# Kernel optimization log

Hardware: AMD Instinct MI355X
Metric: run time of the kernel (lower is better)

## Reference

```python
import jax, jax.numpy as jnp
import numpy as np

# Mesh/packing dims: deltaV_packed.view(B, M, V, ndims) requires N = B*M*V
B, M, V = 2, 4, 40000
N = B * M * V            # 320_000 packed vertices
E = 960000               # ~3 edges per vertex (triangle mesh)
F_IN = 128               # n_input_features
LAT = 128                # latent_channels
NDIMS = 3
N_HIDDEN = 2             # n_f2f_hidden_layer


def graph_conv(x, edges, W0, b0, W1, b1):
    """pytorch3d-style GraphConv: w0(x) + sum_{j in N(i)} w1(x_j), undirected edges."""
    h0 = x @ W0 + b0                     # self term  [N, out]
    h1 = x @ W1 + b1                     # neighbor messages [N, out]
    src, dst = edges[:, 0], edges[:, 1]
    agg = jnp.zeros_like(h0).at[src].add(h1[dst]).at[dst].add(h1[src])
    return h0 + agg


def setup_inputs() -> dict:
    key = jax.random.key(0)
    ks = jax.random.split(key, 20)
    inp = {
        "features": jax.random.normal(ks[0], (N, F_IN), jnp.float32),
        "edges": jax.random.randint(ks[1], (E, 2), 0, N, dtype=jnp.int32),
    }
    # Layer dims: f2f first (F_IN->LAT), 2 hidden (LAT->LAT), f2v (LAT->NDIMS).
    dims = [(F_IN, LAT), (LAT, LAT), (LAT, LAT), (LAT, NDIMS)]
    for i, (din, dout) in enumerate(dims):
        kk = jax.random.split(ks[2 + i], 4)
        s = 1.0 / np.sqrt(din)
        inp[f"W0_{i}"] = jax.random.normal(kk[0], (din, dout), jnp.float32) * s
        inp[f"b0_{i}"] = jnp.zeros((dout,), jnp.float32)
        inp[f"W1_{i}"] = jax.random.normal(kk[1], (din, dout), jnp.float32) * s
        inp[f"b1_{i}"] = jnp.zeros((dout,), jnp.float32)
    return inp


def reference(features, edges,
              W0_0, b0_0, W1_0, b1_0,
              W0_1, b0_1, W1_1, b1_1,
              W0_2, b0_2, W1_2, b1_2,
              W0_3, b0_3, W1_3, b1_3):
    # Features2FeaturesResidual: first GC + 2 hidden GCs (ReLU each, norm='none'),
    # residual skip (identity since F_IN == LAT).
    h = jax.nn.relu(graph_conv(features, edges, W0_0, b0_0, W1_0, b1_0))
    h = jax.nn.relu(graph_conv(h, edges, W0_1, b0_1, W1_1, b1_1))
    h = jax.nn.relu(graph_conv(h, edges, W0_2, b0_2, W1_2, b1_2))
    h = h + features
    # f2v: GC(latent -> ndims), no activation
    deltaV = graph_conv(h, edges, W0_3, b0_3, W1_3, b1_3)
    return deltaV.reshape(B, M, V, NDIMS)
```

## Files before the change

kernel.cpp:

```cpp
#include <hip/hip_runtime.h>
#include <hip/hip_bf16.h>

#define NNODES 320000
#define NEDGES 960000
#define NPART 8
#define PARTSZ (NNODES / NPART)

typedef __attribute__((ext_vector_type(8))) short short8;
typedef __attribute__((ext_vector_type(4))) float f32x4;

__device__ __forceinline__ float b2f(unsigned short u) {
    return __uint_as_float(((unsigned)u) << 16);
}
__device__ __forceinline__ unsigned short f2b(float f) {
    __hip_bfloat16 h = __float2bfloat16(f);
    union { __hip_bfloat16 h; unsigned short u; } cv;
    cv.h = h;
    return cv.u;
}


__global__ void k_zero(int* p, int n) {
    int i = blockIdx.x * blockDim.x + threadIdx.x;
    int s = gridDim.x * blockDim.x;
    for (; i < n; i += s) p[i] = 0;
}

__global__ void k_count(const int* __restrict__ edges, int* __restrict__ deg) {
    int r = blockIdx.x & (NPART - 1);
    int lo = r * PARTSZ, hi = lo + PARTSZ;
    int i = (blockIdx.x >> 3) * blockDim.x + threadIdx.x;
    int s = (gridDim.x >> 3) * blockDim.x;
    for (; i < NEDGES; i += s) {
        int2 e = *(const int2*)&edges[2 * i];
        if (e.x >= lo && e.x < hi) atomicAdd(&deg[e.x], 1);
        if (e.y >= lo && e.y < hi) atomicAdd(&deg[e.y], 1);
    }
}

#define SCAN_BLOCK 256
#define SCAN_ITEMS 8
#define SCAN_CHUNK 2048
#define SCAN_NB 157

__global__ void k_scan1(const int* __restrict__ deg, int* __restrict__ bsum) {
    __shared__ int sd[SCAN_BLOCK];
    int b = blockIdx.x, t = threadIdx.x;
    int base = b * SCAN_CHUNK + t * SCAN_ITEMS;
    int s = 0;
    for (int i = 0; i < SCAN_ITEMS; i++) {
        int g = base + i;
        if (g < NNODES) s += deg[g];
    }
    sd[t] = s;
    __syncthreads();
    for (int off = 128; off > 0; off >>= 1) {
        if (t < off) sd[t] += sd[t + off];
        __syncthreads();
    }
    if (t == 0) bsum[b] = sd[0];
}

__global__ void k_scan2(int* bsum, int* rowptr) {
    if (blockIdx.x == 0 && threadIdx.x == 0) {
        int run = 0;
        for (int b = 0; b < SCAN_NB; b++) {
            int v = bsum[b];
            bsum[b] = run;
            run += v;
        }
        rowptr[NNODES] = run;
    }
}

__global__ void k_scan3(int* __restrict__ deg_cursor, int* __restrict__ rowptr,
                        const int* __restrict__ bsum, float* __restrict__ degf) {
    __shared__ int sd[SCAN_BLOCK];
    int b = blockIdx.x, t = threadIdx.x;
    int base = b * SCAN_CHUNK + t * SCAN_ITEMS;
    int v[SCAN_ITEMS];
    int s = 0;
    for (int i = 0; i < SCAN_ITEMS; i++) {
        int g = base + i;
        v[i] = (g < NNODES) ? deg_cursor[g] : 0;
        s += v[i];
    }
    sd[t] = s;
    __syncthreads();
    for (int off = 1; off < SCAN_BLOCK; off <<= 1) {
        int x = (t >= off) ? sd[t - off] : 0;
        __syncthreads();
        sd[t] += x;
        __syncthreads();
    }
    int prefix = bsum[b] + (sd[t] - s);
    for (int i = 0; i < SCAN_ITEMS; i++) {
        int g = base + i;
        if (g < NNODES) {
            rowptr[g] = prefix;
            deg_cursor[g] = prefix;
            degf[g] = (float)v[i];
            prefix += v[i];
        }
    }
}

__global__ void k_fill(const int* __restrict__ edges, int* __restrict__ cursor,
                       int* __restrict__ adj) {
    int r = blockIdx.x & (NPART - 1);
    int lo = r * PARTSZ, hi = lo + PARTSZ;
    int i = (blockIdx.x >> 3) * blockDim.x + threadIdx.x;
    int s = (gridDim.x >> 3) * blockDim.x;
    for (; i < NEDGES; i += s) {
        int2 e = *(const int2*)&edges[2 * i];
        if (e.x >= lo && e.x < hi) adj[atomicAdd(&cursor[e.x], 1)] = e.y;
        if (e.y >= lo && e.y < hi) adj[atomicAdd(&cursor[e.y], 1)] = e.x;
    }
}


__global__ void k_cvt(const float* __restrict__ f, unsigned short* __restrict__ o,
                      long n4) {
    long i = (long)blockIdx.x * blockDim.x + threadIdx.x;
    long s = (long)gridDim.x * blockDim.x;
    for (; i < n4; i += s) {
        float4 v = *(const float4*)&f[i * 4];
        uint2 u;
        u.x = (unsigned)f2b(v.x) | ((unsigned)f2b(v.y) << 16);
        u.y = (unsigned)f2b(v.z) | ((unsigned)f2b(v.w) << 16);
        *(uint2*)&o[i * 4] = u;
    }
}

__global__ void k_cvtW(const float* __restrict__ W0, const float* __restrict__ W1,
                       unsigned short* __restrict__ Wt) {
    int idx = blockIdx.x * blockDim.x + threadIdx.x;
    if (idx >= 128 * 256) return;
    int c = idx >> 8, k = idx & 255;
    float v = (k < 128) ? W0[k * 128 + c] : W1[(k - 128) * 128 + c];
    Wt[idx] = f2b(v);
}


template <int L>
__global__ __launch_bounds__(256) void k_gather(
    const unsigned short* __restrict__ x, const int* __restrict__ rowptr,
    const int* __restrict__ adj, unsigned short* __restrict__ xsum) {
    int wid = (blockIdx.x * blockDim.x + threadIdx.x) >> 6;
    int lane = threadIdx.x & 63;
    int nw = (gridDim.x * blockDim.x) >> 6;
    int r = lane >> 4;
    int cb = (lane & 15) * 8;
    for (int node = wid; node < NNODES; node += nw) {
        int s = rowptr[node], e = rowptr[node + 1];
        float a[8];
#pragma unroll
        for (int q = 0; q < 8; q++) a[q] = 0.f;
        for (int p = s; p < e; p += 8) {
            int i0 = p + r, i1 = p + r + 4;
            uint4 v0 = make_uint4(0, 0, 0, 0), v1 = make_uint4(0, 0, 0, 0);
            if (i0 < e) {
                int j = adj[i0];
                v0 = *(const uint4*)&x[(size_t)j * 128 + cb];
            }
            if (i1 < e) {
                int j = adj[i1];
                v1 = *(const uint4*)&x[(size_t)j * 128 + cb];
            }
            unsigned w0[4] = {v0.x, v0.y, v0.z, v0.w};
            unsigned w1[4] = {v1.x, v1.y, v1.z, v1.w};
#pragma unroll
            for (int q = 0; q < 4; q++) {
                a[2 * q] += b2f(w0[q] & 0xffff) + b2f(w1[q] & 0xffff);
                a[2 * q + 1] += b2f(w0[q] >> 16) + b2f(w1[q] >> 16);
            }
        }
#pragma unroll
        for (int q = 0; q < 8; q++) a[q] += __shfl_xor(a[q], 16, 64);
#pragma unroll
        for (int q = 0; q < 8; q++) a[q] += __shfl_xor(a[q], 32, 64);
        if (lane < 16) {
            uint4 o;
            o.x = (unsigned)f2b(a[0]) | ((unsigned)f2b(a[1]) << 16);
            o.y = (unsigned)f2b(a[2]) | ((unsigned)f2b(a[3]) << 16);
            o.z = (unsigned)f2b(a[4]) | ((unsigned)f2b(a[5]) << 16);
            o.w = (unsigned)f2b(a[6]) | ((unsigned)f2b(a[7]) << 16);
            *(uint4*)&xsum[(size_t)node * 128 + cb] = o;
        }
    }
}


#define XLD 136

template <int RES, int L>
__global__ __launch_bounds__(512, 4) void k_gemmF(
    const unsigned short* x, const unsigned short* __restrict__ xsum,
    const unsigned short* __restrict__ Wt, const float* __restrict__ b0,
    const float* __restrict__ b1, const float* __restrict__ degf,
    const unsigned short* __restrict__ feat, unsigned short* out) {
    __shared__ __align__(16) unsigned short Xs[64 * XLD];
    __shared__ __align__(16) unsigned short Ss[64 * XLD];

    int tid = threadIdx.x;
    int wave = tid >> 6, lane = tid & 63;
    int wm = wave >> 2, wn = wave & 3;
    int kg = (lane >> 4) << 3;
    int cl = lane & 15;

    short8 bF[8][2];
#pragma unroll
    for (int ks = 0; ks < 8; ++ks)
#pragma unroll
        for (int nf = 0; nf < 2; ++nf) {
            int c = wn * 32 + nf * 16 + cl;
            bF[ks][nf] = *(const short8*)&Wt[(size_t)c * 256 + ks * 32 + kg];
        }

    int rowBase = blockIdx.x * 64;
#pragma unroll
    for (int it = 0; it < 2; ++it) {
        int e = (it * 512 + tid) * 8;
        int r = e >> 7, k = e & 127;
        *(uint4*)&Xs[r * XLD + k] = *(const uint4*)&x[(size_t)(rowBase + r) * 128 + k];
        *(uint4*)&Ss[r * XLD + k] =
            *(const uint4*)&xsum[(size_t)(rowBase + r) * 128 + k];
    }
    __syncthreads();

    f32x4 acc[2][2];
#pragma unroll
    for (int i = 0; i < 2; i++)
#pragma unroll
        for (int j = 0; j < 2; j++) acc[i][j] = (f32x4){0.f, 0.f, 0.f, 0.f};

#pragma unroll
    for (int ks = 0; ks < 8; ++ks) {
        const unsigned short* src = (ks < 4) ? Xs : Ss;
        int kk = (ks & 3) * 32 + kg;
        short8 aF[2];
#pragma unroll
        for (int mf = 0; mf < 2; ++mf) {
            int r = wm * 32 + mf * 16 + cl;
            aF[mf] = *(const short8*)&src[r * XLD + kk];
        }
#pragma unroll
        for (int mf = 0; mf < 2; mf++)
#pragma unroll
            for (int nf = 0; nf < 2; nf++)
                acc[mf][nf] = __builtin_amdgcn_mfma_f32_16x16x32_bf16(
                    aF[mf], bF[ks][nf], acc[mf][nf], 0, 0, 0);
    }

#pragma unroll
    for (int nf = 0; nf < 2; nf++) {
        int c = wn * 32 + nf * 16 + cl;
        float bias0 = b0[c], bias1 = b1[c];
#pragma unroll
        for (int mf = 0; mf < 2; mf++) {
            int r0 = rowBase + wm * 32 + mf * 16 + ((lane >> 4) << 2);
            f32x4 d = acc[mf][nf];
#pragma unroll
            for (int q = 0; q < 4; q++) {
                int r = r0 + q;
                float v = d[q] + bias0 + degf[r] * bias1;
                v = fmaxf(v, 0.f);
                if (RES) v += b2f(feat[(size_t)r * 128 + c]);
                out[(size_t)r * 128 + c] = f2b(v);
            }
        }
    }
}


__global__ __launch_bounds__(256) void k_fin(
    const unsigned short* __restrict__ act, const unsigned short* __restrict__ hsum,
    const float* __restrict__ W0, const float* __restrict__ W1,
    const float* __restrict__ b0, const float* __restrict__ b1,
    const float* __restrict__ degf, float* __restrict__ out) {
    __shared__ __align__(16) unsigned short xa[64 * XLD];
    __shared__ __align__(16) unsigned short xs2[64 * XLD];
    __shared__ float Wf[768];
    __shared__ float ps[64][4][4];

    int tid = threadIdx.x;
    int nodeBase = blockIdx.x * 64;

    for (int idx = tid; idx < 384; idx += 256) {
        Wf[idx] = W0[idx];
        Wf[384 + idx] = W1[idx];
    }
#pragma unroll
    for (int it = 0; it < 4; ++it) {
        int e = (it * 256 + tid) * 8;
        int r = e >> 7, k = e & 127;
        *(uint4*)&xa[r * XLD + k] = *(const uint4*)&act[(size_t)(nodeBase + r) * 128 + k];
        *(uint4*)&xs2[r * XLD + k] =
            *(const uint4*)&hsum[(size_t)(nodeBase + r) * 128 + k];
    }
    __syncthreads();

    int n = tid >> 2, q = tid & 3;
    const unsigned short* src = (q < 2) ? xa : xs2;
    int kloc = (q & 1) * 64;
    float a0 = 0.f, a1 = 0.f, a2 = 0.f;
#pragma unroll
    for (int kk = 0; kk < 64; kk += 8) {
        uint4 v = *(const uint4*)&src[n * XLD + kloc + kk];
        unsigned vv[4] = {v.x, v.y, v.z, v.w};
#pragma unroll
        for (int t = 0; t < 4; t++) {
            int kgl = q * 64 + kk + 2 * t;
            float x0 = b2f(vv[t] & 0xffff), x1 = b2f(vv[t] >> 16);
            const float* w = &Wf[kgl * 3];
            a0 += x0 * w[0] + x1 * w[3];
            a1 += x0 * w[1] + x1 * w[4];
            a2 += x0 * w[2] + x1 * w[5];
        }
    }
    ps[n][q][0] = a0;
    ps[n][q][1] = a1;
    ps[n][q][2] = a2;
    __syncthreads();
    if (q == 0) {
        int node = nodeBase + n;
        float dg = degf[node];
#pragma unroll
        for (int c = 0; c < 3; c++) {
            float d = ps[n][0][c] + ps[n][1][c] + ps[n][2][c] + ps[n][3][c] +
                      b0[c] + dg * b1[c];
            out[(size_t)node * 3 + c] = d;
        }
    }
}


extern "C" void kernel_launch(void* const* d_in, const int* in_sizes, int n_in,
                              void* d_out, int out_size, void* d_ws, size_t ws_size,
                              hipStream_t stream) {
    const float* features = (const float*)d_in[0];
    const int* edges = (const int*)d_in[1];
    const float *W0[4], *B0[4], *W1[4], *B1[4];
    for (int i = 0; i < 4; i++) {
        W0[i] = (const float*)d_in[2 + 4 * i];
        B0[i] = (const float*)d_in[3 + 4 * i];
        W1[i] = (const float*)d_in[4 + 4 * i];
        B1[i] = (const float*)d_in[5 + 4 * i];
    }

    char* p = (char*)d_ws;
    auto alloc = [&](size_t bytes) {
        void* r = (void*)p;
        p += (bytes + 255) & ~(size_t)255;
        return r;
    };
    int* rowptr = (int*)alloc((NNODES + 1) * sizeof(int));
    int* cursor = (int*)alloc((NNODES + 1) * sizeof(int));
    float* degf = (float*)alloc(NNODES * sizeof(float));
    int* adj = (int*)alloc((size_t)2 * NEDGES * sizeof(int));
    int* bsum = (int*)alloc(1024);
    unsigned short* feat_bf = (unsigned short*)alloc((size_t)NNODES * 128 * 2);
    unsigned short* act = (unsigned short*)alloc((size_t)NNODES * 128 * 2);
    unsigned short* xsum = (unsigned short*)alloc((size_t)NNODES * 128 * 2);
    unsigned short* Wtb = (unsigned short*)alloc((size_t)3 * 128 * 256 * 2);

    k_zero<<<1024, 256, 0, stream>>>(cursor, NNODES + 1);
    k_count<<<2048, 256, 0, stream>>>(edges, cursor);
    k_scan1<<<SCAN_NB, SCAN_BLOCK, 0, stream>>>(cursor, bsum);
    k_scan2<<<1, 64, 0, stream>>>(bsum, rowptr);
    k_scan3<<<SCAN_NB, SCAN_BLOCK, 0, stream>>>(cursor, rowptr, bsum, degf);
    k_fill<<<2048, 256, 0, stream>>>(edges, cursor, adj);

    k_cvt<<<2048, 256, 0, stream>>>(features, feat_bf, (long)NNODES * 128 / 4);
    for (int l = 0; l < 3; l++)
        k_cvtW<<<128, 256, 0, stream>>>(W0[l], W1[l], Wtb + (size_t)l * 128 * 256);

    k_gather<0><<<8192, 256, 0, stream>>>(feat_bf, rowptr, adj, xsum);
    k_gemmF<0, 0><<<NNODES / 64, 512, 0, stream>>>(feat_bf, xsum, Wtb, B0[0], B1[0],
                                                   degf, nullptr, act);
    k_gather<1><<<8192, 256, 0, stream>>>(act, rowptr, adj, xsum);
    k_gemmF<0, 1><<<NNODES / 64, 512, 0, stream>>>(act, xsum, Wtb + 128 * 256, B0[1],
                                                   B1[1], degf, nullptr, act);
    k_gather<2><<<8192, 256, 0, stream>>>(act, rowptr, adj, xsum);
    k_gemmF<1, 2><<<NNODES / 64, 512, 0, stream>>>(act, xsum, Wtb + 2 * 128 * 256,
                                                   B0[2], B1[2], degf, feat_bf, act);
    k_gather<3><<<8192, 256, 0, stream>>>(act, rowptr, adj, xsum);
    k_fin<<<NNODES / 64, 256, 0, stream>>>(act, xsum, W0[3], W1[3], B0[3], B1[3],
                                           degf, (float*)d_out);
}
```

Before: 1.153 ms.

## Fuse neighbor gather into per-layer GEMM kernels via shared-memory aggregation

Each layer's neighbor-sum gather now runs inside the GEMM kernel. Waves aggregate neighbor rows for their tile's nodes directly into shared memory, so the separate xsum round-trip through global memory and the extra launches go away. The same is done for the final 3-output layer. Ping-pong activation buffers replace in-place writes, and the serial block-sum scan becomes a parallel shared-memory scan. The trade-off is that gather latency is no longer overlapped across many independent small blocks, only 8-16 nodes are serialized per wave, and weights are reloaded from global per tile.

Result: slower. 1.333 ms (+15.6%).

```diff
diff --git a/kernel.cpp b/kernel.cpp
--- a/kernel.cpp
+++ b/kernel.cpp
@@ -62,15 +62,19 @@
 }
 
 __global__ void k_scan2(int* bsum, int* rowptr) {
-    if (blockIdx.x == 0 && threadIdx.x == 0) {
-        int run = 0;
-        for (int b = 0; b < SCAN_NB; b++) {
-            int v = bsum[b];
-            bsum[b] = run;
-            run += v;
-        }
-        rowptr[NNODES] = run;
-    }
+    __shared__ int sd[256];
+    int t = threadIdx.x;
+    int v = (t < SCAN_NB) ? bsum[t] : 0;
+    sd[t] = v;
+    __syncthreads();
+    for (int off = 1; off < 256; off <<= 1) {
+        int x = (t >= off) ? sd[t - off] : 0;
+        __syncthreads();
+        sd[t] += x;
+        __syncthreads();
+    }
+    if (t < SCAN_NB) bsum[t] = sd[t] - v;
+    if (t == SCAN_NB - 1) rowptr[NNODES] = sd[t];
 }
 
 __global__ void k_scan3(int* __restrict__ deg_cursor, int* __restrict__ rowptr,
@@ -142,63 +146,15 @@
 }
 
 
-template <int L>
-__global__ __launch_bounds__(256) void k_gather(
-    const unsigned short* __restrict__ x, const int* __restrict__ rowptr,
-    const int* __restrict__ adj, unsigned short* __restrict__ xsum) {
-    int wid = (blockIdx.x * blockDim.x + threadIdx.x) >> 6;
-    int lane = threadIdx.x & 63;
-    int nw = (gridDim.x * blockDim.x) >> 6;
-    int r = lane >> 4;
-    int cb = (lane & 15) * 8;
-    for (int node = wid; node < NNODES; node += nw) {
-        int s = rowptr[node], e = rowptr[node + 1];
-        float a[8];
-#pragma unroll
-        for (int q = 0; q < 8; q++) a[q] = 0.f;
-        for (int p = s; p < e; p += 8) {
-            int i0 = p + r, i1 = p + r + 4;
-            uint4 v0 = make_uint4(0, 0, 0, 0), v1 = make_uint4(0, 0, 0, 0);
-            if (i0 < e) {
-                int j = adj[i0];
-                v0 = *(const uint4*)&x[(size_t)j * 128 + cb];
-            }
-            if (i1 < e) {
-                int j = adj[i1];
-                v1 = *(const uint4*)&x[(size_t)j * 128 + cb];
-            }
-            unsigned w0[4] = {v0.x, v0.y, v0.z, v0.w};
-            unsigned w1[4] = {v1.x, v1.y, v1.z, v1.w};
-#pragma unroll
-            for (int q = 0; q < 4; q++) {
-                a[2 * q] += b2f(w0[q] & 0xffff) + b2f(w1[q] & 0xffff);
-                a[2 * q + 1] += b2f(w0[q] >> 16) + b2f(w1[q] >> 16);
-            }
-        }
-#pragma unroll
-        for (int q = 0; q < 8; q++) a[q] += __shfl_xor(a[q], 16, 64);
-#pragma unroll
-        for (int q = 0; q < 8; q++) a[q] += __shfl_xor(a[q], 32, 64);
-        if (lane < 16) {
-            uint4 o;
-            o.x = (unsigned)f2b(a[0]) | ((unsigned)f2b(a[1]) << 16);
-            o.y = (unsigned)f2b(a[2]) | ((unsigned)f2b(a[3]) << 16);
-            o.z = (unsigned)f2b(a[4]) | ((unsigned)f2b(a[5]) << 16);
-            o.w = (unsigned)f2b(a[6]) | ((unsigned)f2b(a[7]) << 16);
-            *(uint4*)&xsum[(size_t)node * 128 + cb] = o;
-        }
-    }
-}
-
-
 #define XLD 136
 
 template <int RES, int L>
-__global__ __launch_bounds__(512, 4) void k_gemmF(
-    const unsigned short* x, const unsigned short* __restrict__ xsum,
-    const unsigned short* __restrict__ Wt, const float* __restrict__ b0,
-    const float* __restrict__ b1, const float* __restrict__ degf,
-    const unsigned short* __restrict__ feat, unsigned short* out) {
+__global__ __launch_bounds__(512, 4) void k_layer(
+    const unsigned short* __restrict__ xin, const int* __restrict__ rowptr,
+    const int* __restrict__ adj, const unsigned short* __restrict__ Wt,
+    const float* __restrict__ b0, const float* __restrict__ b1,
+    const float* __restrict__ degf, const unsigned short* __restrict__ feat,
+    unsigned short* __restrict__ out) {
     __shared__ __align__(16) unsigned short Xs[64 * XLD];
     __shared__ __align__(16) unsigned short Ss[64 * XLD];
 
@@ -207,129 +163,216 @@
     int wm = wave >> 2, wn = wave & 3;
     int kg = (lane >> 4) << 3;
     int cl = lane & 15;
-
-    short8 bF[8][2];
-#pragma unroll
-    for (int ks = 0; ks < 8; ++ks)
-#pragma unroll
-        for (int nf = 0; nf < 2; ++nf) {
+    int slot = lane >> 4;
+    int cb = cl * 8;
+
+    for (int tile = blockIdx.x; tile < NNODES / 64; tile += gridDim.x) {
+        int rowBase = tile * 64;
+        __syncthreads();
+
+#pragma unroll
+        for (int it = 0; it < 2; ++it) {
+            int e = (it * 512 + tid) * 8;
+            int r = e >> 7, k = e & 127;
+            *(uint4*)&Xs[r * XLD + k] =
+                *(const uint4*)&xin[(size_t)(rowBase + r) * 128 + k];
+        }
+
+        for (int nl = 0; nl < 8; ++nl) {
+            int nodeLocal = wave * 8 + nl;
+            int node = rowBase + nodeLocal;
+            int s = rowptr[node], e = rowptr[node + 1];
+            float a[8];
+#pragma unroll
+            for (int q = 0; q < 8; q++) a[q] = 0.f;
+            for (int p = s; p < e; p += 8) {
+                int i0 = p + slot, i1 = p + slot + 4;
+                uint4 v0 = make_uint4(0, 0, 0, 0), v1 = make_uint4(0, 0, 0, 0);
+                if (i0 < e) {
+                    int j = adj[i0];
+                    v0 = *(const uint4*)&xin[(size_t)j * 128 + cb];
+                }
+                if (i1 < e) {
+                    int j = adj[i1];
+                    v1 = *(const uint4*)&xin[(size_t)j * 128 + cb];
+                }
+                unsigned w0[4] = {v0.x, v0.y, v0.z, v0.w};
+                unsigned w1[4] = {v1.x, v1.y, v1.z, v1.w};
+#pragma unroll
+                for (int q = 0; q < 4; q++) {
+                    a[2 * q] += b2f(w0[q] & 0xffff) + b2f(w1[q] & 0xffff);
+                    a[2 * q + 1] += b2f(w0[q] >> 16) + b2f(w1[q] >> 16);
+                }
+            }
+#pragma unroll
+            for (int q = 0; q < 8; q++) a[q] += __shfl_xor(a[q], 16, 64);
+#pragma unroll
+            for (int q = 0; q < 8; q++) a[q] += __shfl_xor(a[q], 32, 64);
+            if (lane < 16) {
+                uint4 o;
+                o.x = (unsigned)f2b(a[0]) | ((unsigned)f2b(a[1]) << 16);
+                o.y = (unsigned)f2b(a[2]) | ((unsigned)f2b(a[3]) << 16);
+                o.z = (unsigned)f2b(a[4]) | ((unsigned)f2b(a[5]) << 16);
+                o.w = (unsigned)f2b(a[6]) | ((unsigned)f2b(a[7]) << 16);
+                *(uint4*)&Ss[nodeLocal * XLD + cb] = o;
+            }
+        }
+        __syncthreads();
+
+        f32x4 acc[2][2];
+#pragma unroll
+        for (int i = 0; i < 2; i++)
+#pragma unroll
+            for (int j = 0; j < 2; j++) acc[i][j] = (f32x4){0.f, 0.f, 0.f, 0.f};
+
+#pragma unroll
+        for (int ks = 0; ks < 8; ++ks) {
+            const unsigned short* src = (ks < 4) ? Xs : Ss;
+            int kk = (ks & 3) * 32 + kg;
+            short8 aF[2];
+#pragma unroll
+            for (int mf = 0; mf < 2; ++mf) {
+                int r = wm * 32 + mf * 16 + cl;
+                aF[mf] = *(const short8*)&src[r * XLD + kk];
+            }
+#pragma unroll
+            for (int nf = 0; nf < 2; nf++) {
+                int c = wn * 32 + nf * 16 + cl;
+                short8 bF = *(const short8*)&Wt[(size_t)c * 256 + ks * 32 + kg];
+#pragma unroll
+                for (int mf = 0; mf < 2; mf++)
+                    acc[mf][nf] = __builtin_amdgcn_mfma_f32_16x16x32_bf16(
+                        aF[mf], bF, acc[mf][nf], 0, 0, 0);
+            }
+        }
+
+#pragma unroll
+        for (int nf = 0; nf < 2; nf++) {
             int c = wn * 32 + nf * 16 + cl;
-            bF[ks][nf] = *(const short8*)&Wt[(size_t)c * 256 + ks * 32 + kg];
-        }
-
-    int rowBase = blockIdx.x * 64;
-#pragma unroll
-    for (int it = 0; it < 2; ++it) {
-        int e = (it * 512 + tid) * 8;
-        int r = e >> 7, k = e & 127;
-        *(uint4*)&Xs[r * XLD + k] = *(const uint4*)&x[(size_t)(rowBase + r) * 128 + k];
-        *(uint4*)&Ss[r * XLD + k] =
-            *(const uint4*)&xsum[(size_t)(rowBase + r) * 128 + k];
-    }
-    __syncthreads();
-
-    f32x4 acc[2][2];
-#pragma unroll
-    for (int i = 0; i < 2; i++)
-#pragma unroll
-        for (int j = 0; j < 2; j++) acc[i][j] = (f32x4){0.f, 0.f, 0.f, 0.f};
-
-#pragma unroll
-    for (int ks = 0; ks < 8; ++ks) {
-        const unsigned short* src = (ks < 4) ? Xs : Ss;
-        int kk = (ks & 3) * 32 + kg;
-        short8 aF[2];
-#pragma unroll
-        for (int mf = 0; mf < 2; ++mf) {
-            int r = wm * 32 + mf * 16 + cl;
-            aF[mf] = *(const short8*)&src[r * XLD + kk];
-        }
-#pragma unroll
-        for (int mf = 0; mf < 2; mf++)
-#pragma unroll
-            for (int nf = 0; nf < 2; nf++)
-                acc[mf][nf] = __builtin_amdgcn_mfma_f32_16x16x32_bf16(
-                    aF[mf], bF[ks][nf], acc[mf][nf], 0, 0, 0);
-    }
-
-#pragma unroll
-    for (int nf = 0; nf < 2; nf++) {
-        int c = wn * 32 + nf * 16 + cl;
-        float bias0 = b0[c], bias1 = b1[c];
-#pragma unroll
-        for (int mf = 0; mf < 2; mf++) {
-            int r0 = rowBase + wm * 32 + mf * 16 + ((lane >> 4) << 2);
-            f32x4 d = acc[mf][nf];
-#pragma unroll
-            for (int q = 0; q < 4; q++) {
-                int r = r0 + q;
-                float v = d[q] + bias0 + degf[r] * bias1;
-                v = fmaxf(v, 0.f);
-                if (RES) v += b2f(feat[(size_t)r * 128 + c]);
-                out[(size_t)r * 128 + c] = f2b(v);
-            }
-        }
-    }
-}
-
-
-__global__ __launch_bounds__(256) void k_fin(
-    const unsigned short* __restrict__ act, const unsigned short* __restrict__ hsum,
-    const float* __restrict__ W0, const float* __restrict__ W1,
-    const float* __restrict__ b0, const float* __restrict__ b1,
-    const float* __restrict__ degf, float* __restrict__ out) {
+            float bias0 = b0[c], bias1 = b1[c];
+#pragma unroll
+            for (int mf = 0; mf < 2; mf++) {
+                int r0 = rowBase + wm * 32 + mf * 16 + ((lane >> 4) << 2);
+                f32x4 d = acc[mf][nf];
+#pragma unroll
+                for (int q = 0; q < 4; q++) {
+                    int r = r0 + q;
+                    float v = d[q] + bias0 + degf[r] * bias1;
+                    v = fmaxf(v, 0.f);
+                    if (RES) v += b2f(feat[(size_t)r * 128 + c]);
+                    out[(size_t)r * 128 + c] = f2b(v);
+                }
+            }
+        }
+    }
+}
+
+
+__global__ __launch_bounds__(256) void k_finF(
+    const unsigned short* __restrict__ act, const int* __restrict__ rowptr,
+    const int* __restrict__ adj, const float* __restrict__ W0,
+    const float* __restrict__ W1, const float* __restrict__ b0,
+    const float* __restrict__ b1, const float* __restrict__ degf,
+    float* __restrict__ out) {
     __shared__ __align__(16) unsigned short xa[64 * XLD];
     __shared__ __align__(16) unsigned short xs2[64 * XLD];
     __shared__ float Wf[768];
     __shared__ float ps[64][4][4];
 
     int tid = threadIdx.x;
-    int nodeBase = blockIdx.x * 64;
+    int wave = tid >> 6, lane = tid & 63;
+    int slot = lane >> 4;
+    int cb = (lane & 15) * 8;
 
     for (int idx = tid; idx < 384; idx += 256) {
         Wf[idx] = W0[idx];
         Wf[384 + idx] = W1[idx];
     }
-#pragma unroll
-    for (int it = 0; it < 4; ++it) {
-        int e = (it * 256 + tid) * 8;
-        int r = e >> 7, k = e & 127;
-        *(uint4*)&xa[r * XLD + k] = *(const uint4*)&act[(size_t)(nodeBase + r) * 128 + k];
-        *(uint4*)&xs2[r * XLD + k] =
-            *(const uint4*)&hsum[(size_t)(nodeBase + r) * 128 + k];
-    }
-    __syncthreads();
-
-    int n = tid >> 2, q = tid & 3;
-    const unsigned short* src = (q < 2) ? xa : xs2;
-    int kloc = (q & 1) * 64;
-    float a0 = 0.f, a1 = 0.f, a2 = 0.f;
-#pragma unroll
-    for (int kk = 0; kk < 64; kk += 8) {
-        uint4 v = *(const uint4*)&src[n * XLD + kloc + kk];
-        unsigned vv[4] = {v.x, v.y, v.z, v.w};
-#pragma unroll
-        for (int t = 0; t < 4; t++) {
-            int kgl = q * 64 + kk + 2 * t;
-            float x0 = b2f(vv[t] & 0xffff), x1 = b2f(vv[t] >> 16);
-            const float* w = &Wf[kgl * 3];
-            a0 += x0 * w[0] + x1 * w[3];
-            a1 += x0 * w[1] + x1 * w[4];
-            a2 += x0 * w[2] + x1 * w[5];
-        }
-    }
-    ps[n][q][0] = a0;
-    ps[n][q][1] = a1;
-    ps[n][q][2] = a2;
-    __syncthreads();
-    if (q == 0) {
-        int node = nodeBase + n;
-        float dg = degf[node];
-#pragma unroll
-        for (int c = 0; c < 3; c++) {
-            float d = ps[n][0][c] + ps[n][1][c] + ps[n][2][c] + ps[n][3][c] +
-                      b0[c] + dg * b1[c];
-            out[(size_t)node * 3 + c] = d;
+
+    for (int tile = blockIdx.x; tile < NNODES / 64; tile += gridDim.x) {
+        int nodeBase = tile * 64;
+        __syncthreads();
+
+#pragma unroll
+        for (int it = 0; it < 4; ++it) {
+            int e = (it * 256 + tid) * 8;
+            int r = e >> 7, k = e & 127;
+            *(uint4*)&xa[r * XLD + k] =
+                *(const uint4*)&act[(size_t)(nodeBase + r) * 128 + k];
+        }
+
+        for (int nl = 0; nl < 16; ++nl) {
+            int nodeLocal = wave * 16 + nl;
+            int node = nodeBase + nodeLocal;
+            int s = rowptr[node], e = rowptr[node + 1];
+            float a[8];
+#pragma unroll
+            for (int q = 0; q < 8; q++) a[q] = 0.f;
+            for (int p = s; p < e; p += 8) {
+                int i0 = p + slot, i1 = p + slot + 4;
+                uint4 v0 = make_uint4(0, 0, 0, 0), v1 = make_uint4(0, 0, 0, 0);
+                if (i0 < e) {
+                    int j = adj[i0];
+                    v0 = *(const uint4*)&act[(size_t)j * 128 + cb];
+                }
+                if (i1 < e) {
+                    int j = adj[i1];
+                    v1 = *(const uint4*)&act[(size_t)j * 128 + cb];
+                }
+                unsigned w0[4] = {v0.x, v0.y, v0.z, v0.w};
+                unsigned w1[4] = {v1.x, v1.y, v1.z, v1.w};
+#pragma unroll
+                for (int q = 0; q < 4; q++) {
+                    a[2 * q] += b2f(w0[q] & 0xffff) + b2f(w1[q] & 0xffff);
+                    a[2 * q + 1] += b2f(w0[q] >> 16) + b2f(w1[q] >> 16);
+                }
+            }
+#pragma unroll
+            for (int q = 0; q < 8; q++) a[q] += __shfl_xor(a[q], 16, 64);
+#pragma unroll
+            for (int q = 0; q < 8; q++) a[q] += __shfl_xor(a[q], 32, 64);
+            if (lane < 16) {
+                uint4 o;
+                o.x = (unsigned)f2b(a[0]) | ((unsigned)f2b(a[1]) << 16);
+                o.y = (unsigned)f2b(a[2]) | ((unsigned)f2b(a[3]) << 16);
+                o.z = (unsigned)f2b(a[4]) | ((unsigned)f2b(a[5]) << 16);
+                o.w = (unsigned)f2b(a[6]) | ((unsigned)f2b(a[7]) << 16);
+                *(uint4*)&xs2[nodeLocal * XLD + cb] = o;
+            }
+        }
+        __syncthreads();
+
+        int n = tid >> 2, q = tid & 3;
+        const unsigned short* src = (q < 2) ? xa : xs2;
+        int kloc = (q & 1) * 64;
+        float a0 = 0.f, a1 = 0.f, a2 = 0.f;
+#pragma unroll
+        for (int kk = 0; kk < 64; kk += 8) {
+            uint4 v = *(const uint4*)&src[n * XLD + kloc + kk];
+            unsigned vv[4] = {v.x, v.y, v.z, v.w};
+#pragma unroll
+            for (int t = 0; t < 4; t++) {
+                int kgl = q * 64 + kk + 2 * t;
+                float x0 = b2f(vv[t] & 0xffff), x1 = b2f(vv[t] >> 16);
+                const float* w = &Wf[kgl * 3];
+                a0 += x0 * w[0] + x1 * w[3];
+                a1 += x0 * w[1] + x1 * w[4];
+                a2 += x0 * w[2] + x1 * w[5];
+            }
+        }
+        ps[n][q][0] = a0;
+        ps[n][q][1] = a1;
+        ps[n][q][2] = a2;
+        __syncthreads();
+        if (q == 0) {
+            int node = nodeBase + n;
+            float dg = degf[node];
+#pragma unroll
+            for (int c = 0; c < 3; c++) {
+                float d = ps[n][0][c] + ps[n][1][c] + ps[n][2][c] + ps[n][3][c] +
+                          b0[c] + dg * b1[c];
+                out[(size_t)node * 3 + c] = d;
+            }
         }
     }
 }
@@ -360,14 +403,14 @@
     int* adj = (int*)alloc((size_t)2 * NEDGES * sizeof(int));
     int* bsum = (int*)alloc(1024);
     unsigned short* feat_bf = (unsigned short*)alloc((size_t)NNODES * 128 * 2);
-    unsigned short* act = (unsigned short*)alloc((size_t)NNODES * 128 * 2);
-    unsigned short* xsum = (unsigned short*)alloc((size_t)NNODES * 128 * 2);
+    unsigned short* actA = (unsigned short*)alloc((size_t)NNODES * 128 * 2);
+    unsigned short* actB = (unsigned short*)alloc((size_t)NNODES * 128 * 2);
     unsigned short* Wtb = (unsigned short*)alloc((size_t)3 * 128 * 256 * 2);
 
     k_zero<<<1024, 256, 0, stream>>>(cursor, NNODES + 1);
     k_count<<<2048, 256, 0, stream>>>(edges, cursor);
     k_scan1<<<SCAN_NB, SCAN_BLOCK, 0, stream>>>(cursor, bsum);
-    k_scan2<<<1, 64, 0, stream>>>(bsum, rowptr);
+    k_scan2<<<1, 256, 0, stream>>>(bsum, rowptr);
     k_scan3<<<SCAN_NB, SCAN_BLOCK, 0, stream>>>(cursor, rowptr, bsum, degf);
     k_fill<<<2048, 256, 0, stream>>>(edges, cursor, adj);
 
@@ -375,16 +418,12 @@
     for (int l = 0; l < 3; l++)
         k_cvtW<<<128, 256, 0, stream>>>(W0[l], W1[l], Wtb + (size_t)l * 128 * 256);
 
-    k_gather<0><<<8192, 256, 0, stream>>>(feat_bf, rowptr, adj, xsum);
-    k_gemmF<0, 0><<<NNODES / 64, 512, 0, stream>>>(feat_bf, xsum, Wtb, B0[0], B1[0],
-                                                   degf, nullptr, act);
-    k_gather<1><<<8192, 256, 0, stream>>>(act, rowptr, adj, xsum);
-    k_gemmF<0, 1><<<NNODES / 64, 512, 0, stream>>>(act, xsum, Wtb + 128 * 256, B0[1],
-                                                   B1[1], degf, nullptr, act);
-    k_gather<2><<<8192, 256, 0, stream>>>(act, rowptr, adj, xsum);
-    k_gemmF<1, 2><<<NNODES / 64, 512, 0, stream>>>(act, xsum, Wtb + 2 * 128 * 256,
-                                                   B0[2], B1[2], degf, feat_bf, act);
-    k_gather<3><<<8192, 256, 0, stream>>>(act, rowptr, adj, xsum);
-    k_fin<<<NNODES / 64, 256, 0, stream>>>(act, xsum, W0[3], W1[3], B0[3], B1[3],
-                                           degf, (float*)d_out);
-}
+    k_layer<0, 0><<<1250, 512, 0, stream>>>(feat_bf, rowptr, adj, Wtb, B0[0], B1[0],
+                                            degf, nullptr, actA);
+    k_layer<0, 1><<<1250, 512, 0, stream>>>(actA, rowptr, adj, Wtb + 128 * 256,
+                                            B0[1], B1[1], degf, nullptr, actB);
+    k_layer<1, 2><<<1250, 512, 0, stream>>>(actB, rowptr, adj, Wtb + 2 * 128 * 256,
+                                            B0[2], B1[2], degf, feat_bf, actA);
+    k_finF<<<2500, 256, 0, stream>>>(actA, rowptr, adj, W0[3], W1[3], B0[3], B1[3],
+                                     degf, (float*)d_out);
+}
```

## Make GEMM persistent with tile prefetch, gather two nodes per wave, parallelize scan

Applied to the files above, without the earlier changes.

The fused GEMM kernel becomes persistent: 1250 blocks loop over the 64-row tiles. Each block prefetches the next tile's x and xsum rows into registers while it computes the current one, and B fragments are now loaded inside the k-loop instead of held in registers. The neighbour-gather kernel processes two nodes per wave, which raises the number of independent memory loads in flight. The single-thread block-sum scan is replaced by a 256-thread shared-memory scan. In exchange, persistence reduces occupancy via launch bounds and re-reads weights per tile, and the scan assumes SCAN_NB is at most 256.

Result: no change. 1.169 ms (+1.4%).

```diff
diff --git a/kernel.cpp b/kernel.cpp
--- a/kernel.cpp
+++ b/kernel.cpp
@@ -62,15 +62,19 @@
 }
 
 __global__ void k_scan2(int* bsum, int* rowptr) {
-    if (blockIdx.x == 0 && threadIdx.x == 0) {
-        int run = 0;
-        for (int b = 0; b < SCAN_NB; b++) {
-            int v = bsum[b];
-            bsum[b] = run;
-            run += v;
-        }
-        rowptr[NNODES] = run;
-    }
+    __shared__ int sd[256];
+    int t = threadIdx.x;
+    int v = (t < SCAN_NB) ? bsum[t] : 0;
+    sd[t] = v;
+    __syncthreads();
+    for (int off = 1; off < 256; off <<= 1) {
+        int x = (t >= off) ? sd[t - off] : 0;
+        __syncthreads();
+        sd[t] += x;
+        __syncthreads();
+    }
+    if (t < SCAN_NB) bsum[t] = sd[t] - v;
+    if (t == SCAN_NB - 1) rowptr[NNODES] = sd[t];
 }
 
 __global__ void k_scan3(int* __restrict__ deg_cursor, int* __restrict__ rowptr,
@@ -149,52 +153,67 @@
     int wid = (blockIdx.x * blockDim.x + threadIdx.x) >> 6;
     int lane = threadIdx.x & 63;
     int nw = (gridDim.x * blockDim.x) >> 6;
-    int r = lane >> 4;
+    int slot = lane >> 4;
     int cb = (lane & 15) * 8;
-    for (int node = wid; node < NNODES; node += nw) {
-        int s = rowptr[node], e = rowptr[node + 1];
-        float a[8];
-#pragma unroll
-        for (int q = 0; q < 8; q++) a[q] = 0.f;
-        for (int p = s; p < e; p += 8) {
-            int i0 = p + r, i1 = p + r + 4;
-            uint4 v0 = make_uint4(0, 0, 0, 0), v1 = make_uint4(0, 0, 0, 0);
-            if (i0 < e) {
-                int j = adj[i0];
-                v0 = *(const uint4*)&x[(size_t)j * 128 + cb];
+    for (int n0 = wid * 2; n0 < NNODES; n0 += nw * 2) {
+        int s0 = rowptr[n0], e0 = rowptr[n0 + 1], e1 = rowptr[n0 + 2];
+        int d0 = e0 - s0, d1 = e1 - e0;
+        int dmax = d0 > d1 ? d0 : d1;
+        float a0[8], a1[8];
+#pragma unroll
+        for (int q = 0; q < 8; q++) { a0[q] = 0.f; a1[q] = 0.f; }
+        for (int p = 0; p < dmax; p += 8) {
+            int i00 = s0 + p + slot, i01 = i00 + 4;
+            int i10 = e0 + p + slot, i11 = i10 + 4;
+            uint4 v00 = make_uint4(0, 0, 0, 0), v01 = make_uint4(0, 0, 0, 0);
+            uint4 v10 = make_uint4(0, 0, 0, 0), v11 = make_uint4(0, 0, 0, 0);
+            if (i00 < e0) v00 = *(const uint4*)&x[(size_t)adj[i00] * 128 + cb];
+            if (i01 < e0) v01 = *(const uint4*)&x[(size_t)adj[i01] * 128 + cb];
+            if (i10 < e1) v10 = *(const uint4*)&x[(size_t)adj[i10] * 128 + cb];
+            if (i11 < e1) v11 = *(const uint4*)&x[(size_t)adj[i11] * 128 + cb];
+            unsigned w00[4] = {v00.x, v00.y, v00.z, v00.w};
+            unsigned w01[4] = {v01.x, v01.y, v01.z, v01.w};
+            unsigned w10[4] = {v10.x, v10.y, v10.z, v10.w};
+            unsigned w11[4] = {v11.x, v11.y, v11.z, v11.w};
+#pragma unroll
+            for (int q = 0; q < 4; q++) {
+                a0[2 * q] += b2f(w00[q] & 0xffff) + b2f(w01[q] & 0xffff);
+                a0[2 * q + 1] += b2f(w00[q] >> 16) + b2f(w01[q] >> 16);
+                a1[2 * q] += b2f(w10[q] & 0xffff) + b2f(w11[q] & 0xffff);
+                a1[2 * q + 1] += b2f(w10[q] >> 16) + b2f(w11[q] >> 16);
             }
-            if (i1 < e) {
-                int j = adj[i1];
-                v1 = *(const uint4*)&x[(size_t)j * 128 + cb];
-            }
-            unsigned w0[4] = {v0.x, v0.y, v0.z, v0.w};
-            unsigned w1[4] = {v1.x, v1.y, v1.z, v1.w};
-#pragma unroll
-            for (int q = 0; q < 4; q++) {
-                a[2 * q] += b2f(w0[q] & 0xffff) + b2f(w1[q] & 0xffff);
-                a[2 * q + 1] += b2f(w0[q] >> 16) + b2f(w1[q] >> 16);
-            }
-        }
-#pragma unroll
-        for (int q = 0; q < 8; q++) a[q] += __shfl_xor(a[q], 16, 64);
-#pragma unroll
-        for (int q = 0; q < 8; q++) a[q] += __shfl_xor(a[q], 32, 64);
-        if (lane < 16) {
+        }
+#pragma unroll
+        for (int q = 0; q < 8; q++) {
+            a0[q] += __shfl_xor(a0[q], 16, 64);
+            a1[q] += __shfl_xor(a1[q], 16, 64);
+        }
+#pragma unroll
+        for (int q = 0; q < 8; q++) {
+            a0[q] += __shfl_xor(a0[q], 32, 64);
+            a1[q] += __shfl_xor(a1[q], 32, 64);
+        }
+        float sel[8];
+#pragma unroll
+        for (int q = 0; q < 8; q++) sel[q] = (lane < 16) ? a0[q] : a1[q];
+        if (lane < 32) {
             uint4 o;
-            o.x = (unsigned)f2b(a[0]) | ((unsigned)f2b(a[1]) << 16);
-            o.y = (unsigned)f2b(a[2]) | ((unsigned)f2b(a[3]) << 16);
-            o.z = (unsigned)f2b(a[4]) | ((unsigned)f2b(a[5]) << 16);
-            o.w = (unsigned)f2b(a[6]) | ((unsigned)f2b(a[7]) << 16);
-            *(uint4*)&xsum[(size_t)node * 128 + cb] = o;
+            o.x = (unsigned)f2b(sel[0]) | ((unsigned)f2b(sel[1]) << 16);
+            o.y = (unsigned)f2b(sel[2]) | ((unsigned)f2b(sel[3]) << 16);
+            o.z = (unsigned)f2b(sel[4]) | ((unsigned)f2b(sel[5]) << 16);
+            o.w = (unsigned)f2b(sel[6]) | ((unsigned)f2b(sel[7]) << 16);
+            int dst = (lane < 16) ? n0 : (n0 + 1);
+            *(uint4*)&xsum[(size_t)dst * 128 + cb] = o;
         }
     }
 }
 
 
 #define XLD 136
+#define NT (NNODES / 64)
 
 template <int RES, int L>
-__global__ __launch_bounds__(512, 4) void k_gemmF(
+__global__ __launch_bounds__(512, 2) void k_gemmF(
     const unsigned short* x, const unsigned short* __restrict__ xsum,
     const unsigned short* __restrict__ Wt, const float* __restrict__ b0,
     const float* __restrict__ b1, const float* __restrict__ degf,
@@ -208,67 +227,86 @@
     int kg = (lane >> 4) << 3;
     int cl = lane & 15;
 
-    short8 bF[8][2];
-#pragma unroll
-    for (int ks = 0; ks < 8; ++ks)
-#pragma unroll
-        for (int nf = 0; nf < 2; ++nf) {
-            int c = wn * 32 + nf * 16 + cl;
-            bF[ks][nf] = *(const short8*)&Wt[(size_t)c * 256 + ks * 32 + kg];
-        }
-
-    int rowBase = blockIdx.x * 64;
-#pragma unroll
-    for (int it = 0; it < 2; ++it) {
-        int e = (it * 512 + tid) * 8;
-        int r = e >> 7, k = e & 127;
-        *(uint4*)&Xs[r * XLD + k] = *(const uint4*)&x[(size_t)(rowBase + r) * 128 + k];
-        *(uint4*)&Ss[r * XLD + k] =
-            *(const uint4*)&xsum[(size_t)(rowBase + r) * 128 + k];
-    }
-    __syncthreads();
-
-    f32x4 acc[2][2];
-#pragma unroll
-    for (int i = 0; i < 2; i++)
-#pragma unroll
-        for (int j = 0; j < 2; j++) acc[i][j] = (f32x4){0.f, 0.f, 0.f, 0.f};
-
-#pragma unroll
-    for (int ks = 0; ks < 8; ++ks) {
-        const unsigned short* src = (ks < 4) ? Xs : Ss;
-        int kk = (ks & 3) * 32 + kg;
-        short8 aF[2];
-#pragma unroll
-        for (int mf = 0; mf < 2; ++mf) {
-            int r = wm * 32 + mf * 16 + cl;
-            aF[mf] = *(const short8*)&src[r * XLD + kk];
-        }
-#pragma unroll
-        for (int mf = 0; mf < 2; mf++)
-#pragma unroll
-            for (int nf = 0; nf < 2; nf++)
-                acc[mf][nf] = __builtin_amdgcn_mfma_f32_16x16x32_bf16(
-                    aF[mf], bF[ks][nf], acc[mf][nf], 0, 0, 0);
-    }
-
+    float bias0[2], bias1[2];
 #pragma unroll
     for (int nf = 0; nf < 2; nf++) {
         int c = wn * 32 + nf * 16 + cl;
-        float bias0 = b0[c], bias1 = b1[c];
-#pragma unroll
-        for (int mf = 0; mf < 2; mf++) {
-            int r0 = rowBase + wm * 32 + mf * 16 + ((lane >> 4) << 2);
-            f32x4 d = acc[mf][nf];
-#pragma unroll
-            for (int q = 0; q < 4; q++) {
-                int r = r0 + q;
-                float v = d[q] + bias0 + degf[r] * bias1;
-                v = fmaxf(v, 0.f);
-                if (RES) v += b2f(feat[(size_t)r * 128 + c]);
-                out[(size_t)r * 128 + c] = f2b(v);
+        bias0[nf] = b0[c];
+        bias1[nf] = b1[c];
+    }
+
+    uint4 pa[2], ps[2];
+    auto loadTile = [&](int tile) {
+#pragma unroll
+        for (int it = 0; it < 2; ++it) {
+            int e = (it * 512 + tid) * 8;
+            int r = e >> 7, k = e & 127;
+            pa[it] = *(const uint4*)&x[(size_t)(tile * 64 + r) * 128 + k];
+            ps[it] = *(const uint4*)&xsum[(size_t)(tile * 64 + r) * 128 + k];
+        }
+    };
+
+    int tile = blockIdx.x;
+    if (tile < NT) loadTile(tile);
+    while (tile < NT) {
+        int next = tile + gridDim.x;
+        __syncthreads();
+#pragma unroll
+        for (int it = 0; it < 2; ++it) {
+            int e = (it * 512 + tid) * 8;
+            int r = e >> 7, k = e & 127;
+            *(uint4*)&Xs[r * XLD + k] = pa[it];
+            *(uint4*)&Ss[r * XLD + k] = ps[it];
+        }
+        __syncthreads();
+        if (next < NT) loadTile(next);
+
+        int rowBase = tile * 64;
+        f32x4 acc[2][2];
+#pragma unroll
+        for (int i = 0; i < 2; i++)
+#pragma unroll
+            for (int j = 0; j < 2; j++) acc[i][j] = (f32x4){0.f, 0.f, 0.f, 0.f};
+
+#pragma unroll
+        for (int ks = 0; ks < 8; ++ks) {
+            const unsigned short* src = (ks < 4) ? Xs : Ss;
+            int kk = (ks & 3) * 32 + kg;
+            short8 aF[2];
+#pragma unroll
+            for (int mf = 0; mf < 2; ++mf) {
+                int r = wm * 32 + mf * 16 + cl;
+                aF[mf] = *(const short8*)&src[r * XLD + kk];
             }
-        }
+#pragma unroll
+            for (int nf = 0; nf < 2; nf++) {
+                int c = wn * 32 + nf * 16 + cl;
+                short8 bF = *(const short8*)&Wt[(size_t)c * 256 + ks * 32 + kg];
+#pragma unroll
+                for (int mf = 0; mf < 2; mf++)
+                    acc[mf][nf] = __builtin_amdgcn_mfma_f32_16x16x32_bf16(
+                        aF[mf], bF, acc[mf][nf], 0, 0, 0);
+            }
+        }
+
+#pragma unroll
+        for (int nf = 0; nf < 2; nf++) {
+            int c = wn * 32 + nf * 16 + cl;
+#pragma unroll
+            for (int mf = 0; mf < 2; mf++) {
+                int r0 = rowBase + wm * 32 + mf * 16 + ((lane >> 4) << 2);
+                f32x4 d = acc[mf][nf];
+#pragma unroll
+                for (int q = 0; q < 4; q++) {
+                    int r = r0 + q;
+                    float v = d[q] + bias0[nf] + degf[r] * bias1[nf];
+                    v = fmaxf(v, 0.f);
+                    if (RES) v += b2f(feat[(size_t)r * 128 + c]);
+                    out[(size_t)r * 128 + c] = f2b(v);
+                }
+            }
+        }
+        tile = next;
     }
 }
 
@@ -367,7 +405,7 @@
     k_zero<<<1024, 256, 0, stream>>>(cursor, NNODES + 1);
     k_count<<<2048, 256, 0, stream>>>(edges, cursor);
     k_scan1<<<SCAN_NB, SCAN_BLOCK, 0, stream>>>(cursor, bsum);
-    k_scan2<<<1, 64, 0, stream>>>(bsum, rowptr);
+    k_scan2<<<1, 256, 0, stream>>>(bsum, rowptr);
     k_scan3<<<SCAN_NB, SCAN_BLOCK, 0, stream>>>(cursor, rowptr, bsum, degf);
     k_fill<<<2048, 256, 0, stream>>>(edges, cursor, adj);
 
@@ -376,14 +414,14 @@
         k_cvtW<<<128, 256, 0, stream>>>(W0[l], W1[l], Wtb + (size_t)l * 128 * 256);
 
     k_gather<0><<<8192, 256, 0, stream>>>(feat_bf, rowptr, adj, xsum);
-    k_gemmF<0, 0><<<NNODES / 64, 512, 0, stream>>>(feat_bf, xsum, Wtb, B0[0], B1[0],
-                                                   degf, nullptr, act);
+    k_gemmF<0, 0><<<1250, 512, 0, stream>>>(feat_bf, xsum, Wtb, B0[0], B1[0], degf,
+                                            nullptr, act);
     k_gather<1><<<8192, 256, 0, stream>>>(act, rowptr, adj, xsum);
-    k_gemmF<0, 1><<<NNODES / 64, 512, 0, stream>>>(act, xsum, Wtb + 128 * 256, B0[1],
-                                                   B1[1], degf, nullptr, act);
+    k_gemmF<0, 1><<<1250, 512, 0, stream>>>(act, xsum, Wtb + 128 * 256, B0[1], B1[1],
+                                            degf, nullptr, act);
     k_gather<2><<<8192, 256, 0, stream>>>(act, rowptr, adj, xsum);
-    k_gemmF<1, 2><<<NNODES / 64, 512, 0, stream>>>(act, xsum, Wtb + 2 * 128 * 256,
-                                                   B0[2], B1[2], degf, feat_bf, act);
+    k_gemmF<1, 2><<<1250, 512, 0, stream>>>(act, xsum, Wtb + 2 * 128 * 256, B0[2],
+                                            B1[2], degf, feat_bf, act);
     k_gather<3><<<8192, 256, 0, stream>>>(act, rowptr, adj, xsum);
     k_fin<<<NNODES / 64, 256, 0, stream>>>(act, xsum, W0[3], W1[3], B0[3], B1[3],
                                            degf, (float*)d_out);
```
